# Performance work log

Hardware: AMD Instinct MI355X
Metric: run time of the kernel (lower is better)

## Reference

```python
import jax, jax.numpy as jnp
import numpy as np

TOP_K = 2
EPS = 1e-6

def setup_inputs() -> dict:
    B, S, H, G, E, M = 2, 2048, 1024, 256, 8, 2048
    key = jax.random.key(0)
    ks = jax.random.split(key, 16)
    s_h = 1.0 / np.sqrt(H)
    s_g = 1.0 / np.sqrt(G)
    s_m = 1.0 / np.sqrt(M)
    return {
        "x": jax.random.normal(ks[0], (B, S, H), jnp.float32),
        "genre_embed": jax.random.normal(ks[1], (B, 1, G), jnp.float32),
        "rms_w": jnp.ones((H,), jnp.float32),
        "wg_W": jax.random.normal(ks[2], (H, E), jnp.float32) * s_h,
        "wg_b": jnp.zeros((E,), jnp.float32),
        "gg_W": jax.random.normal(ks[3], (G, E), jnp.float32) * s_g,
        "gg_b": jnp.zeros((E,), jnp.float32),
        "W1": jax.random.normal(ks[4], (E, H, M), jnp.float32) * s_h,
        "b1": jnp.zeros((E, M), jnp.float32),
        "W2": jax.random.normal(ks[5], (E, M, M), jnp.float32) * s_m,
        "b2": jnp.zeros((E, M), jnp.float32),
        "W3": jax.random.normal(ks[6], (E, M, H), jnp.float32) * s_m,
        "b3": jnp.zeros((E, H), jnp.float32),
    }


def reference(x, genre_embed, rms_w, wg_W, wg_b, gg_W, gg_b, W1, b1, W2, b2, W3, b3):
    E = W1.shape[0]
    # RMSNorm
    var = jnp.mean(x * x, axis=-1, keepdims=True)
    xn = rms_w * (x * jax.lax.rsqrt(var + EPS))
    # gating: word gate [B,S,E] + genre gate [B,1,E] (broadcast over seq)
    gate = (xn @ wg_W + wg_b) + (genre_embed @ gg_W + gg_b)
    gate_w = jax.nn.softmax(gate, axis=-1)
    topk_w, topk_i = jax.lax.top_k(gate_w, TOP_K)  # [B,S,K]
    # combine weights per expert: sum_k topk_w * onehot(topk_i)
    cw = jnp.sum(jax.nn.one_hot(topk_i, E, dtype=x.dtype) * topk_w[..., None], axis=-2)  # [B,S,E]
    # dense all-expert MLP (equivalent math to masked dispatch/combine)
    h1 = jax.nn.relu(jnp.einsum('bsh,ehm->bsem', x, W1) + b1)
    h2 = jax.nn.relu(jnp.einsum('bsem,emn->bsen', h1, W2) + b2)
    out_e = jnp.einsum('bsen,enh->bseh', h2, W3) + b3
    return jnp.einsum('bseh,bse->bsh', out_e, cw)
```

## Files before the change

### kernel.cpp

```cpp
#include <hip/hip_runtime.h>
#include <hip/hip_bf16.h>

#define T_TOK 4096
#define N_PAIR 8192
#define H_DIM 1024
#define M_DIM 2048
#define E_NUM 8

#define T_W1 2048
#define T_W2 4096
#define T_W3 2048
#define T_ROUT 1024

using bf16x8 = __attribute__((ext_vector_type(8))) short;
using f32x4  = __attribute__((ext_vector_type(4))) float;

__device__ __forceinline__ unsigned short f2bf(float f) {
    unsigned int u = __builtin_bit_cast(unsigned int, f);
    u += 0x7fffu + ((u >> 16) & 1u);
    return (unsigned short)(u >> 16);
}
__device__ __forceinline__ float bf2f(unsigned short u) {
    return __builtin_bit_cast(float, (unsigned int)u << 16);
}

__device__ __forceinline__ void async16(const unsigned short* g, unsigned short* l) {
    __builtin_amdgcn_global_load_lds(
        (const __attribute__((address_space(1))) void*)g,
        (__attribute__((address_space(3))) void*)l, 16, 0, 0);
}

__global__ void k_prep(const float* __restrict__ W1, const float* __restrict__ W2,
                       const float* __restrict__ W3,
                       unsigned short* __restrict__ W1t, unsigned short* __restrict__ W2t,
                       unsigned short* __restrict__ W3t,
                       const float* __restrict__ x, const float* __restrict__ rms_w,
                       const float* __restrict__ wg_W, const float* __restrict__ genre,
                       const float* __restrict__ gg_W, const float* __restrict__ gg_b,
                       const float* __restrict__ wg_b,
                       int* __restrict__ tok_e, float* __restrict__ tok_w)
{
    __shared__ float ld[64][132];
    int bid = blockIdx.x;

    if (bid < T_W1 + T_W2 + T_W3) {
        const float* W; unsigned short* Wt; int tile, kshift, ntshift, N, K;
        if (bid < T_W1)              { W = W1; Wt = W1t; tile = bid;                 K = H_DIM; N = M_DIM; kshift = 10; ntshift = 4; }
        else if (bid < T_W1 + T_W2)  { W = W2; Wt = W2t; tile = bid - T_W1;          K = M_DIM; N = M_DIM; kshift = 11; ntshift = 4; }
        else                         { W = W3; Wt = W3t; tile = bid - T_W1 - T_W2;   K = M_DIM; N = H_DIM; kshift = 11; ntshift = 3; }
        int r0 = (tile >> ntshift) * 64;
        int n0 = (tile & ((1 << ntshift) - 1)) * 128;
        int t = threadIdx.x;
        {
            int rr = t >> 2, c0 = t & 3;
            const float4* src = (const float4*)(W + (size_t)(r0 + rr) * N + n0);
#pragma unroll
            for (int cc = 0; cc < 8; cc++) {
                float4 v = src[c0 + cc * 4];
                float* d = &ld[rr][(c0 + cc * 4) * 4];
                d[0] = v.x; d[1] = v.y; d[2] = v.z; d[3] = v.w;
            }
        }
        __syncthreads();
        {
            int n = t >> 1, khalf = t & 1;
            int kb = khalf * 32;
            int e = r0 >> kshift;
            int kloc = (r0 & (K - 1)) + kb;
            unsigned short* dst = Wt + ((size_t)e * N + (n0 + n)) * K + kloc;
#pragma unroll
            for (int blk = 0; blk < 4; blk++) {
                bf16x8 o;
#pragma unroll
                for (int q = 0; q < 8; q++) o[q] = (short)f2bf(ld[kb + blk * 8 + q][n]);
                *(bf16x8*)(dst + blk * 8) = o;
            }
        }
        return;
    }

    int wave = threadIdx.x >> 6, lane = threadIdx.x & 63;
    int tok = (bid - (T_W1 + T_W2 + T_W3)) * 4 + wave;
    int b = tok >> 11;
    const float* xr = x + (size_t)tok * H_DIM;
    float xv[16];
    float ss = 0.f;
#pragma unroll
    for (int j = 0; j < 16; j++) { xv[j] = xr[lane + 64 * j]; ss += xv[j] * xv[j]; }
#pragma unroll
    for (int off = 32; off > 0; off >>= 1) ss += __shfl_xor(ss, off);
    float rstd = rsqrtf(ss * (1.f / 1024.f) + 1e-6f);
    float g[8] = {0.f, 0.f, 0.f, 0.f, 0.f, 0.f, 0.f, 0.f};
#pragma unroll
    for (int gi0 = 0; gi0 < 4; gi0++) {
        int gi = lane + gi0 * 64;
        float gf = genre[b * 256 + gi];
        const float4* w4 = (const float4*)(gg_W + gi * 8);
        float4 wa = w4[0], wb = w4[1];
        g[0] += gf * wa.x; g[1] += gf * wa.y; g[2] += gf * wa.z; g[3] += gf * wa.w;
        g[4] += gf * wb.x; g[5] += gf * wb.y; g[6] += gf * wb.z; g[7] += gf * wb.w;
    }
#pragma unroll
    for (int j = 0; j < 16; j++) {
        int h = lane + 64 * j;
        float xn = xv[j] * rstd * rms_w[h];
        const float4* w4 = (const float4*)(wg_W + h * 8);
        float4 wa = w4[0], wb = w4[1];
        g[0] += xn * wa.x; g[1] += xn * wa.y; g[2] += xn * wa.z; g[3] += xn * wa.w;
        g[4] += xn * wb.x; g[5] += xn * wb.y; g[6] += xn * wb.z; g[7] += xn * wb.w;
    }
#pragma unroll
    for (int e = 0; e < 8; e++) {
#pragma unroll
        for (int off = 32; off > 0; off >>= 1) g[e] += __shfl_xor(g[e], off);
    }
    if (lane == 0) {
#pragma unroll
        for (int e = 0; e < 8; e++) g[e] += wg_b[e] + gg_b[e];
        float m = g[0];
        for (int e = 1; e < 8; e++) m = fmaxf(m, g[e]);
        float p[8], psum = 0.f;
        for (int e = 0; e < 8; e++) { p[e] = expf(g[e] - m); psum += p[e]; }
        int i0 = 0;
        for (int e = 1; e < 8; e++) if (p[e] > p[i0]) i0 = e;
        int i1 = (i0 == 0) ? 1 : 0;
        for (int e = 0; e < 8; e++) if (e != i0 && p[e] > p[i1]) i1 = e;
        float inv = 1.f / psum;
        tok_e[tok * 2] = i0;         tok_e[tok * 2 + 1] = i1;
        tok_w[tok * 2] = p[i0] * inv; tok_w[tok * 2 + 1] = p[i1] * inv;
    }
}

__global__ void k_scan(const int* __restrict__ tok_e, int* __restrict__ meta)
{
    __shared__ int cnt[8];
    int t = threadIdx.x;
    if (t < 8) cnt[t] = 0;
    __syncthreads();
    for (int p = t; p < N_PAIR; p += 256) atomicAdd(&cnt[tok_e[p]], 1);
    __syncthreads();
    if (t == 0) {
        int acc = 0;
        for (int e = 0; e < 8; e++) {
            meta[e] = cnt[e]; meta[8 + e] = acc; meta[16 + e] = acc; acc += cnt[e];
        }
    }
}

__global__ void k_gather(const float* __restrict__ x, const int* __restrict__ tok_e,
                         int* __restrict__ meta, int* __restrict__ pair_pos,
                         unsigned short* __restrict__ x_g)
{
    int wave = threadIdx.x >> 6, lane = threadIdx.x & 63;
    int p = blockIdx.x * 4 + wave;
    int t = p >> 1;
    int e = tok_e[p];
    int pos;
    if (lane == 0) {
        pos = atomicAdd(&meta[16 + e], 1);
        pair_pos[p] = pos;
    }
    pos = __shfl(pos, 0);
    const float4* src = (const float4*)(x + (size_t)t * H_DIM);
    ushort4* dst = (ushort4*)(x_g + (size_t)pos * H_DIM);
#pragma unroll
    for (int j = 0; j < 4; j++) {
        float4 v = src[lane + 64 * j];
        ushort4 o;
        o.x = f2bf(v.x); o.y = f2bf(v.y); o.z = f2bf(v.z); o.w = f2bf(v.w);
        dst[lane + 64 * j] = o;
    }
}

template<bool RELU>
__global__ void k_gemm(const unsigned short* __restrict__ A,
                       const unsigned short* __restrict__ Wt,
                       const float* __restrict__ bias,
                       unsigned short* __restrict__ C,
                       const int* __restrict__ meta,
                       int K, int N)
{
    int e = blockIdx.z;
    int cnt = meta[e];
    int by = blockIdx.y;
    if (by * 128 >= cnt) return;
    int base = meta[8 + e];
    int bx = blockIdx.x;

    __shared__ __align__(16) unsigned short As[128 * 64];
    __shared__ __align__(16) unsigned short Bs[128 * 64];

    int tid = threadIdx.x;
    int wave = tid >> 6, lane = tid & 63;
    int lrow8 = lane >> 3;
    int lslot = lane & 7;
    int chunk_g = (lslot ^ lrow8) * 8;

    const unsigned short* Bw = Wt + (size_t)e * N * K + (size_t)(bx * 128) * K;
    const unsigned short* gA[4]; const unsigned short* gB[4];
    unsigned short* lA[4]; unsigned short* lB[4];
#pragma unroll
    for (int c = 0; c < 4; c++) {
        int rloc = wave * 32 + c * 8 + lrow8;
        int ra = base + by * 128 + rloc;
        ra = min(ra, N_PAIR - 1);
        gA[c] = A + (size_t)ra * K + chunk_g;
        gB[c] = Bw + (size_t)rloc * K + chunk_g;
        lA[c] = &As[(wave * 32 + c * 8) * 64];
        lB[c] = &Bs[(wave * 32 + c * 8) * 64];
    }

    int wr = (wave >> 1) * 64, wc = (wave & 1) * 64;
    int lm = lane & 15, lq = lane >> 4;

    int aoff[4][2], boff[4][2];
#pragma unroll
    for (int i = 0; i < 4; i++)
#pragma unroll
        for (int h = 0; h < 2; h++) {
            int R = wr + i * 16 + lm;
            aoff[i][h] = R * 64 + (((h * 4 + lq) ^ (R & 7)) * 8);
            int Nn = wc + i * 16 + lm;
            boff[i][h] = Nn * 64 + (((h * 4 + lq) ^ (Nn & 7)) * 8);
        }

    f32x4 acc[4][4] = {};

    for (int kt = 0; kt < K; kt += 64) {
#pragma unroll
        for (int c = 0; c < 4; c++) { async16(gA[c] + kt, lA[c]); async16(gB[c] + kt, lB[c]); }
        __syncthreads();
#pragma unroll
        for (int h = 0; h < 2; h++) {
            bf16x8 af[4], bfr[4];
#pragma unroll
            for (int i = 0; i < 4; i++) af[i] = *(const bf16x8*)&As[aoff[i][h]];
#pragma unroll
            for (int j = 0; j < 4; j++) bfr[j] = *(const bf16x8*)&Bs[boff[j][h]];
#pragma unroll
            for (int i = 0; i < 4; i++)
#pragma unroll
                for (int j = 0; j < 4; j++)
                    acc[i][j] = __builtin_amdgcn_mfma_f32_16x16x32_bf16(af[i], bfr[j], acc[i][j], 0, 0, 0);
        }
        __syncthreads();
    }

#pragma unroll
    for (int j = 0; j < 4; j++) {
        int n = bx * 128 + wc + j * 16 + lm;
        float bv = bias[(size_t)e * N + n];
#pragma unroll
        for (int i = 0; i < 4; i++) {
#pragma unroll
            for (int r = 0; r < 4; r++) {
                int grow = by * 128 + wr + i * 16 + lq * 4 + r;
                if (grow < cnt) {
                    float v = acc[i][j][r] + bv;
                    if (RELU) v = fmaxf(v, 0.f);
                    C[(size_t)(base + grow) * N + n] = f2bf(v);
                }
            }
        }
    }
}

__global__ void k_combine(const unsigned short* __restrict__ o3,
                          const int* __restrict__ pair_pos,
                          const float* __restrict__ tok_w, float* __restrict__ out)
{
    int t = blockIdx.x;
    int c = threadIdx.x;
    int p0 = pair_pos[t * 2], p1 = pair_pos[t * 2 + 1];
    float w0 = tok_w[t * 2], w1 = tok_w[t * 2 + 1];
    ushort4 a = ((const ushort4*)(o3 + (size_t)p0 * H_DIM))[c];
    ushort4 bq = ((const ushort4*)(o3 + (size_t)p1 * H_DIM))[c];
    float4 o;
    o.x = w0 * bf2f(a.x) + w1 * bf2f(bq.x);
    o.y = w0 * bf2f(a.y) + w1 * bf2f(bq.y);
    o.z = w0 * bf2f(a.z) + w1 * bf2f(bq.z);
    o.w = w0 * bf2f(a.w) + w1 * bf2f(bq.w);
    ((float4*)(out + (size_t)t * H_DIM))[c] = o;
}

extern "C" void kernel_launch(void* const* d_in, const int* in_sizes, int n_in,
                              void* d_out, int out_size, void* d_ws, size_t ws_size,
                              hipStream_t stream) {
    const float* x      = (const float*)d_in[0];
    const float* genre  = (const float*)d_in[1];
    const float* rms_w  = (const float*)d_in[2];
    const float* wg_W   = (const float*)d_in[3];
    const float* wg_b   = (const float*)d_in[4];
    const float* gg_W   = (const float*)d_in[5];
    const float* gg_b   = (const float*)d_in[6];
    const float* W1     = (const float*)d_in[7];
    const float* b1     = (const float*)d_in[8];
    const float* W2     = (const float*)d_in[9];
    const float* b2     = (const float*)d_in[10];
    const float* W3     = (const float*)d_in[11];
    const float* b3     = (const float*)d_in[12];
    float* out = (float*)d_out;

    char* p = (char*)d_ws;
    auto alloc = [&](size_t bytes) { char* r = p; p += (bytes + 255) & ~(size_t)255; return r; };
    unsigned short* W1t = (unsigned short*)alloc((size_t)E_NUM * H_DIM * M_DIM * 2);
    unsigned short* W2t = (unsigned short*)alloc((size_t)E_NUM * M_DIM * M_DIM * 2);
    unsigned short* W3t = (unsigned short*)alloc((size_t)E_NUM * M_DIM * H_DIM * 2);
    unsigned short* x_g = (unsigned short*)alloc((size_t)N_PAIR * H_DIM * 2);
    unsigned short* h1  = (unsigned short*)alloc((size_t)N_PAIR * M_DIM * 2);
    unsigned short* h2  = (unsigned short*)alloc((size_t)N_PAIR * M_DIM * 2);
    unsigned short* o3  = (unsigned short*)alloc((size_t)N_PAIR * H_DIM * 2);
    int*   meta         = (int*)alloc(24 * 4);
    int*   tok_e        = (int*)alloc((size_t)N_PAIR * 4);
    float* tok_w        = (float*)alloc((size_t)N_PAIR * 4);
    int*   pair_pos     = (int*)alloc((size_t)N_PAIR * 4);

    dim3 blk(256);

    k_prep<<<T_W1 + T_W2 + T_W3 + T_ROUT, blk, 0, stream>>>(
        W1, W2, W3, W1t, W2t, W3t, x, rms_w, wg_W, genre, gg_W, gg_b, wg_b,
        tok_e, tok_w);
    k_scan<<<1, blk, 0, stream>>>(tok_e, meta);
    k_gather<<<N_PAIR / 4, blk, 0, stream>>>(x, tok_e, meta, pair_pos, x_g);

    k_gemm<true ><<<dim3(M_DIM / 128, 32, E_NUM), blk, 0, stream>>>(
        x_g, W1t, b1, h1, meta, H_DIM, M_DIM);
    k_gemm<true ><<<dim3(M_DIM / 128, 32, E_NUM), blk, 0, stream>>>(
        h1, W2t, b2, h2, meta, M_DIM, M_DIM);
    k_gemm<false><<<dim3(H_DIM / 128, 32, E_NUM), blk, 0, stream>>>(
        h2, W3t, b3, o3, meta, M_DIM, H_DIM);

    k_combine<<<T_TOK, blk, 0, stream>>>(o3, pair_pos, tok_w, out);

    (void)in_sizes; (void)n_in; (void)ws_size;
}
```

Measured before the change: 694.4 us.

## Triple-buffer GEMM K-loop with async prefetch two tiles ahead

Replaces the single-buffered 64-wide K loop with a three-stage ring of 32-wide LDS tiles. Global-to-LDS async loads for tile t+2 are issued before computing tile t, and explicit vmcnt waits plus barriers replace the full syncthreads pairs. The goal is to hide global load latency behind MFMA work. The cost is more barriers per unit of K, hand-tuned vmcnt counts that depend on how many loads each stage issues, and a new XOR swizzle for the narrower tiles.

Result: slower. 714.8 us (+2.9%).

```diff
diff --git a/kernel.cpp b/kernel.cpp
--- a/kernel.cpp
+++ b/kernel.cpp
@@ -187,64 +187,89 @@
     int base = meta[8 + e];
     int bx = blockIdx.x;
 
-    __shared__ __align__(16) unsigned short As[128 * 64];
-    __shared__ __align__(16) unsigned short Bs[128 * 64];
+    __shared__ __align__(16) unsigned short AsF[3 * 128 * 32];
+    __shared__ __align__(16) unsigned short BsF[3 * 128 * 32];
 
     int tid = threadIdx.x;
     int wave = tid >> 6, lane = tid & 63;
-    int lrow8 = lane >> 3;
-    int lslot = lane & 7;
-    int chunk_g = (lslot ^ lrow8) * 8;
+    int lrow = lane >> 2;
+    int chunk_g = ((lane & 3) ^ (lrow & 3)) * 8;
 
     const unsigned short* Bw = Wt + (size_t)e * N * K + (size_t)(bx * 128) * K;
-    const unsigned short* gA[4]; const unsigned short* gB[4];
-    unsigned short* lA[4]; unsigned short* lB[4];
-#pragma unroll
-    for (int c = 0; c < 4; c++) {
-        int rloc = wave * 32 + c * 8 + lrow8;
+    const unsigned short* gA[2]; const unsigned short* gB[2];
+    int sAB[2];
+#pragma unroll
+    for (int c = 0; c < 2; c++) {
+        int rloc = wave * 32 + c * 16 + lrow;
         int ra = base + by * 128 + rloc;
         ra = min(ra, N_PAIR - 1);
         gA[c] = A + (size_t)ra * K + chunk_g;
         gB[c] = Bw + (size_t)rloc * K + chunk_g;
-        lA[c] = &As[(wave * 32 + c * 8) * 64];
-        lB[c] = &Bs[(wave * 32 + c * 8) * 64];
+        sAB[c] = (wave * 32 + c * 16) * 32;
     }
 
     int wr = (wave >> 1) * 64, wc = (wave & 1) * 64;
     int lm = lane & 15, lq = lane >> 4;
 
-    int aoff[4][2], boff[4][2];
-#pragma unroll
-    for (int i = 0; i < 4; i++)
-#pragma unroll
-        for (int h = 0; h < 2; h++) {
-            int R = wr + i * 16 + lm;
-            aoff[i][h] = R * 64 + (((h * 4 + lq) ^ (R & 7)) * 8);
-            int Nn = wc + i * 16 + lm;
-            boff[i][h] = Nn * 64 + (((h * 4 + lq) ^ (Nn & 7)) * 8);
-        }
+    int aoff[4], boff[4];
+#pragma unroll
+    for (int i = 0; i < 4; i++) {
+        int R = wr + i * 16 + lm;
+        aoff[i] = R * 32 + ((lq ^ (R & 3)) * 8);
+        int Nn = wc + i * 16 + lm;
+        boff[i] = Nn * 32 + ((lq ^ (Nn & 3)) * 8);
+    }
 
     f32x4 acc[4][4] = {};
 
-    for (int kt = 0; kt < K; kt += 64) {
-#pragma unroll
-        for (int c = 0; c < 4; c++) { async16(gA[c] + kt, lA[c]); async16(gB[c] + kt, lB[c]); }
-        __syncthreads();
-#pragma unroll
-        for (int h = 0; h < 2; h++) {
-            bf16x8 af[4], bfr[4];
-#pragma unroll
-            for (int i = 0; i < 4; i++) af[i] = *(const bf16x8*)&As[aoff[i][h]];
-#pragma unroll
-            for (int j = 0; j < 4; j++) bfr[j] = *(const bf16x8*)&Bs[boff[j][h]];
-#pragma unroll
-            for (int i = 0; i < 4; i++)
-#pragma unroll
-                for (int j = 0; j < 4; j++)
-                    acc[i][j] = __builtin_amdgcn_mfma_f32_16x16x32_bf16(af[i], bfr[j], acc[i][j], 0, 0, 0);
-        }
-        __syncthreads();
-    }
+#define STAGE(sb, T)                                                          \
+    {                                                                         \
+        _Pragma("unroll")                                                     \
+        for (int c = 0; c < 2; c++) {                                         \
+            async16(gA[c] + (T) * 32, &AsF[(sb) * 4096 + sAB[c]]);            \
+            async16(gB[c] + (T) * 32, &BsF[(sb) * 4096 + sAB[c]]);            \
+        }                                                                     \
+    }
+
+#define COMPUTE(cb)                                                           \
+    {                                                                         \
+        const unsigned short* Ab = &AsF[(cb) * 4096];                         \
+        const unsigned short* Bb = &BsF[(cb) * 4096];                         \
+        bf16x8 af[4], bfr[4];                                                 \
+        _Pragma("unroll")                                                     \
+        for (int i = 0; i < 4; i++) af[i] = *(const bf16x8*)&Ab[aoff[i]];     \
+        _Pragma("unroll")                                                     \
+        for (int j = 0; j < 4; j++) bfr[j] = *(const bf16x8*)&Bb[boff[j]];    \
+        _Pragma("unroll")                                                     \
+        for (int i = 0; i < 4; i++)                                           \
+            _Pragma("unroll")                                                 \
+            for (int j = 0; j < 4; j++)                                       \
+                acc[i][j] = __builtin_amdgcn_mfma_f32_16x16x32_bf16(af[i], bfr[j], acc[i][j], 0, 0, 0); \
+    }
+
+    int nt = K >> 5;
+
+    STAGE(0, 0);
+    STAGE(1, 1);
+
+    int sb = 2, cb = 0;
+#pragma unroll 1
+    for (int t = 0; t <= nt - 3; ++t) {
+        STAGE(sb, t + 2);
+        sb = (sb == 2) ? 0 : sb + 1;
+        asm volatile("s_waitcnt vmcnt(8)\n\ts_barrier" ::: "memory");
+        COMPUTE(cb);
+        cb = (cb == 2) ? 0 : cb + 1;
+        asm volatile("s_barrier" ::: "memory");
+    }
+    asm volatile("s_waitcnt vmcnt(4)\n\ts_barrier" ::: "memory");
+    COMPUTE(cb);
+    cb = (cb == 2) ? 0 : cb + 1;
+    asm volatile("s_waitcnt vmcnt(0)\n\ts_barrier" ::: "memory");
+    COMPUTE(cb);
+
+#undef STAGE
+#undef COMPUTE
 
 #pragma unroll
     for (int j = 0; j < 4; j++) {
```

## Overlap next K-tile global-to-LDS loads with MFMA compute in grouped GEMM

Applied to the files above, without the earlier changes.

Restructures the GEMM main loop so each K-tile's fragments are read from LDS into registers first. After a barrier, the async global-to-LDS copy for the next tile is issued before the MFMA block, so memory traffic overlaps compute within a single LDS buffer. It also adds launch bounds for two blocks per CU and raises wave priority around the MFMA section. More live fragment registers and the occupancy bound could cause spills or scheduling pressure.

After: 676.8 us. 2.5% less time.

```diff
diff --git a/kernel.cpp b/kernel.cpp
--- a/kernel.cpp
+++ b/kernel.cpp
@@ -173,12 +173,13 @@
 }
 
 template<bool RELU>
-__global__ void k_gemm(const unsigned short* __restrict__ A,
-                       const unsigned short* __restrict__ Wt,
-                       const float* __restrict__ bias,
-                       unsigned short* __restrict__ C,
-                       const int* __restrict__ meta,
-                       int K, int N)
+__global__ __launch_bounds__(256, 2)
+void k_gemm(const unsigned short* __restrict__ A,
+            const unsigned short* __restrict__ Wt,
+            const float* __restrict__ bias,
+            unsigned short* __restrict__ C,
+            const int* __restrict__ meta,
+            int K, int N)
 {
     int e = blockIdx.z;
     int cnt = meta[e];
@@ -226,24 +227,43 @@
 
     f32x4 acc[4][4] = {};
 
+    {
+#pragma unroll
+        for (int c = 0; c < 4; c++) { async16(gA[c], lA[c]); async16(gB[c], lB[c]); }
+        asm volatile("s_waitcnt vmcnt(0)" ::: "memory");
+        __builtin_amdgcn_s_barrier();
+    }
+
+#pragma unroll 1
     for (int kt = 0; kt < K; kt += 64) {
-#pragma unroll
-        for (int c = 0; c < 4; c++) { async16(gA[c] + kt, lA[c]); async16(gB[c] + kt, lB[c]); }
-        __syncthreads();
+        bf16x8 af[4][2], bfr[4][2];
 #pragma unroll
         for (int h = 0; h < 2; h++) {
-            bf16x8 af[4], bfr[4];
-#pragma unroll
-            for (int i = 0; i < 4; i++) af[i] = *(const bf16x8*)&As[aoff[i][h]];
-#pragma unroll
-            for (int j = 0; j < 4; j++) bfr[j] = *(const bf16x8*)&Bs[boff[j][h]];
+#pragma unroll
+            for (int i = 0; i < 4; i++) af[i][h]  = *(const bf16x8*)&As[aoff[i][h]];
+#pragma unroll
+            for (int j = 0; j < 4; j++) bfr[j][h] = *(const bf16x8*)&Bs[boff[j][h]];
+        }
+        asm volatile("s_waitcnt lgkmcnt(0)" ::: "memory");
+        __builtin_amdgcn_s_barrier();
+        if (kt + 64 < K) {
+#pragma unroll
+            for (int c = 0; c < 4; c++) { async16(gA[c] + kt + 64, lA[c]); async16(gB[c] + kt + 64, lB[c]); }
+        }
+        __builtin_amdgcn_sched_barrier(0);
+        __builtin_amdgcn_s_setprio(1);
+#pragma unroll
+        for (int h = 0; h < 2; h++)
 #pragma unroll
             for (int i = 0; i < 4; i++)
 #pragma unroll
                 for (int j = 0; j < 4; j++)
-                    acc[i][j] = __builtin_amdgcn_mfma_f32_16x16x32_bf16(af[i], bfr[j], acc[i][j], 0, 0, 0);
-        }
-        __syncthreads();
+                    acc[i][j] = __builtin_amdgcn_mfma_f32_16x16x32_bf16(af[i][h], bfr[j][h], acc[i][j], 0, 0, 0);
+        __builtin_amdgcn_s_setprio(0);
+        if (kt + 64 < K) {
+            asm volatile("s_waitcnt vmcnt(0)" ::: "memory");
+            __builtin_amdgcn_s_barrier();
+        }
     }
 
 #pragma unroll
```
